# Optimization experiments

Measured on AMD Instinct MI355X. Metric: run time of the kernel, lower is better.

The kernel has to match this reference:

```python
import jax, jax.numpy as jnp
import numpy as np

B, T, C, H, E, K = 4, 2048, 1024, 2048, 8, 2


def setup_inputs() -> dict:
    key = jax.random.key(0)
    ks = jax.random.split(key, 9)
    s = lambda k, shape, fan: jax.random.normal(k, shape, jnp.float32) / np.sqrt(fan)
    return {
        "x": jax.random.normal(ks[0], (B, T, C), jnp.float32),
        "gate_w": s(ks[1], (C, E), C),            # router gate (no bias)
        "sg_w": s(ks[2], (C, H), C),              # shared expert: gate proj
        "su_w": s(ks[3], (C, H), C),              # shared expert: up proj
        "sd_w": s(ks[4], (H, C), H),              # shared expert: down proj
        "eg_w": s(ks[5], (E, C, H), C),           # routed experts: gate proj
        "eu_w": s(ks[6], (E, C, H), C),           # routed experts: up proj
        "ed_w": s(ks[7], (E, H, C), H),           # routed experts: down proj
    }


def _swiglu(x, wg, wu, wd):
    # x: (B,T,C) -> (B,T,C)
    return jnp.einsum("bth,hc->btc", jax.nn.silu(jnp.einsum("btc,ch->bth", x, wg)) * jnp.einsum("btc,ch->bth", x, wu), wd)


def reference(x, gate_w, sg_w, su_w, sd_w, eg_w, eu_w, ed_w):
    # Router: top-k over expert logits, softmax over selected logits
    logits = jnp.einsum("btc,ce->bte", x, gate_w)            # (B,T,E)
    topk_logits, topk_idx = jax.lax.top_k(logits, K)         # (B,T,K)
    weights = jax.nn.softmax(topk_logits, axis=-1)           # (B,T,K)
    # Dense per-expert combine weight: w_e[b,t,e] = sum_k weights*(idx==e)
    onehot = jax.nn.one_hot(topk_idx, E, dtype=x.dtype)      # (B,T,K,E)
    dense_w = jnp.einsum("btk,btke->bte", weights, onehot)   # (B,T,E)

    shared_out = _swiglu(x, sg_w, su_w, sd_w)

    # Scan over experts (small fixed E), accumulating weighted expert outputs.
    dense_w_e = jnp.moveaxis(dense_w, -1, 0)                 # (E,B,T)

    def step(acc, params):
        wg, wu, wd, w = params
        return acc + w[..., None] * _swiglu(x, wg, wu, wd), None

    expert_out, _ = jax.lax.scan(step, jnp.zeros_like(x), (eg_w, eu_w, ed_w, dense_w_e))
    return shared_out + expert_out, logits
```

## Files before the change

kernel.cpp:

```cpp
#include <hip/hip_runtime.h>
#include <cstdint>
#include <cstddef>

#define NTOK 8192
#define CDIM 1024
#define HDIM 2048
#define NEXP 8
#define NSEG 9
#define MAXTILES 104
#define GUTILES (MAXTILES * 2)

typedef __bf16 bf16;
typedef unsigned short u16;
typedef __attribute__((ext_vector_type(8))) __bf16 bf16x8;
typedef __attribute__((ext_vector_type(4))) float f32x4;

__device__ __forceinline__ u16 f2bf(float f) {
  union { u16 u; __bf16 b; } cv;
  cv.b = (__bf16)f;
  return cv.u;
}

__device__ __forceinline__ void gload_lds16(const bf16* g, bf16* l) {
  __builtin_amdgcn_global_load_lds(
      (const __attribute__((address_space(1))) unsigned int*)g,
      (__attribute__((address_space(3))) unsigned int*)l, 16, 0, 0);
}

__global__ __launch_bounds__(64) void init_kernel(int* __restrict__ counts,
                                                  int* __restrict__ fill) {
  if (threadIdx.x < NEXP) {
    counts[threadIdx.x] = 0;
    fill[threadIdx.x] = 0;
  }
}

__global__ __launch_bounds__(256) void zero_out_kernel(float* __restrict__ out) {
  size_t i = ((size_t)blockIdx.x * 256 + threadIdx.x) * 8;
  float4 z = {0.f, 0.f, 0.f, 0.f};
  *(float4*)(out + i) = z;
  *(float4*)(out + i + 4) = z;
}

__global__ __launch_bounds__(256) void cast_x_kernel(
    const float* __restrict__ src, bf16* __restrict__ dst) {
  size_t i = ((size_t)blockIdx.x * 256 + threadIdx.x) * 8;
  float4 a = *(const float4*)(src + i);
  float4 b = *(const float4*)(src + i + 4);
  bf16x8 p;
  p[0] = (bf16)a.x; p[1] = (bf16)a.y; p[2] = (bf16)a.z; p[3] = (bf16)a.w;
  p[4] = (bf16)b.x; p[5] = (bf16)b.y; p[6] = (bf16)b.z; p[7] = (bf16)b.w;
  *(bf16x8*)(dst + i) = p;
}

__global__ __launch_bounds__(256) void router2_kernel(
    const float* __restrict__ x, const float* __restrict__ gw,
    float* __restrict__ logits_out, int* __restrict__ tk_e,
    float* __restrict__ tk_w, int* __restrict__ counts) {
  int wv = threadIdx.x >> 6, l = threadIdx.x & 63;
  int t = blockIdx.x * 4 + wv;
  const float* xr = x + (size_t)t * CDIM;
  float acc[NEXP];
#pragma unroll
  for (int e = 0; e < NEXP; ++e) acc[e] = 0.f;
  for (int c = l; c < CDIM; c += 64) {
    float xv = xr[c];
    const float* g = gw + (size_t)c * NEXP;
    float4 g0 = *(const float4*)(g);
    float4 g1 = *(const float4*)(g + 4);
    acc[0] += xv * g0.x; acc[1] += xv * g0.y; acc[2] += xv * g0.z; acc[3] += xv * g0.w;
    acc[4] += xv * g1.x; acc[5] += xv * g1.y; acc[6] += xv * g1.z; acc[7] += xv * g1.w;
  }
#pragma unroll
  for (int off = 32; off > 0; off >>= 1) {
#pragma unroll
    for (int e = 0; e < NEXP; ++e) acc[e] += __shfl_xor(acc[e], off, 64);
  }
  int e0 = 0; float l0 = acc[0];
#pragma unroll
  for (int e = 1; e < NEXP; ++e) { if (acc[e] > l0) { l0 = acc[e]; e0 = e; } }
  int e1 = -1; float l1 = -3.4e38f;
#pragma unroll
  for (int e = 0; e < NEXP; ++e) { if (e != e0 && acc[e] > l1) { l1 = acc[e]; e1 = e; } }
  float ex = expf(l1 - l0);
  float w0 = 1.f / (1.f + ex), w1 = ex / (1.f + ex);
  if (l < NEXP) logits_out[(size_t)t * NEXP + l] = acc[l];
  if (l == 0) {
    tk_e[2 * t] = e0; tk_e[2 * t + 1] = e1;
    tk_w[2 * t] = w0; tk_w[2 * t + 1] = w1;
    atomicAdd(&counts[e0], 1);
    atomicAdd(&counts[e1], 1);
  }
}

__global__ __launch_bounds__(256) void offsets_kernel(
    const int* __restrict__ counts, int* __restrict__ offs_g,
    int* __restrict__ tile_seg, int* __restrict__ list_tok,
    float* __restrict__ w_row) {
  __shared__ int off[NSEG], pad[NSEG], cnt[NSEG], ntot;
  int tid = threadIdx.x;
  if (tid == 0) {
    int tot = 0;
    for (int e = 0; e < NSEG; ++e) {
      int c = (e < NEXP) ? counts[e] : NTOK;
      cnt[e] = c; off[e] = tot;
      int p = (c + 255) & ~255;
      pad[e] = p; tot += p;
    }
    ntot = tot;
  }
  __syncthreads();
  if (tid < NSEG) offs_g[tid] = off[tid];
  for (int gt = tid; gt < MAXTILES; gt += 256) {
    int row = gt * 256, seg = -1;
    if (row < ntot) {
      for (int e = 0; e < NSEG; ++e)
        if (row >= off[e] && row < off[e] + pad[e]) { seg = e; break; }
    }
    tile_seg[gt] = seg;
  }
  for (int e = 0; e < NSEG; ++e)
    for (int i = off[e] + cnt[e] + tid; i < off[e] + pad[e]; i += 256) {
      list_tok[i] = 0;
      w_row[i] = 0.f;
    }
}

__global__ __launch_bounds__(256) void scatter_kernel(
    const int* __restrict__ tk_e, const float* __restrict__ tk_w,
    const int* __restrict__ offs, int* __restrict__ fill,
    int* __restrict__ list_tok, float* __restrict__ w_row) {
  int t = blockIdx.x * 256 + threadIdx.x;
  int e0 = tk_e[2 * t], e1 = tk_e[2 * t + 1];
  float w0 = tk_w[2 * t], w1 = tk_w[2 * t + 1];
  int p0 = atomicAdd(&fill[e0], 1);
  int i0 = offs[e0] + p0;
  list_tok[i0] = t; w_row[i0] = w0;
  int p1 = atomicAdd(&fill[e1], 1);
  int i1 = offs[e1] + p1;
  list_tok[i1] = t; w_row[i1] = w1;
  int rsh = offs[NEXP] + t;
  list_tok[rsh] = t; w_row[rsh] = 1.f;
}

__device__ __forceinline__ void transpose_body(const float* __restrict__ src,
                                               u16* __restrict__ dst, int R, int C) {
  __shared__ u16 tile[64][65];
  int r0 = blockIdx.y * 64, c0 = blockIdx.x * 64;
  int tr = threadIdx.x >> 2;
  int tc = (threadIdx.x & 3) * 16;
  const float* s = src + (size_t)(r0 + tr) * C + c0 + tc;
  float4 f[4];
#pragma unroll
  for (int q = 0; q < 4; ++q) f[q] = *(const float4*)(s + q * 4);
#pragma unroll
  for (int q = 0; q < 4; ++q) {
    tile[tr][tc + q * 4 + 0] = f2bf(f[q].x);
    tile[tr][tc + q * 4 + 1] = f2bf(f[q].y);
    tile[tr][tc + q * 4 + 2] = f2bf(f[q].z);
    tile[tr][tc + q * 4 + 3] = f2bf(f[q].w);
  }
  __syncthreads();
  union { uint4 v[2]; u16 e[16]; } u;
#pragma unroll
  for (int j = 0; j < 16; ++j) u.e[j] = tile[tc + j][tr];
  u16* d = dst + (size_t)(c0 + tr) * R + r0 + tc;
  *(uint4*)d = u.v[0];
  *(uint4*)(d + 8) = u.v[1];
}

__global__ __launch_bounds__(256) void transpose_cast_kernel(
    const float* __restrict__ src, u16* __restrict__ dst, int R, int C) {
  transpose_body(src, dst, R, C);
}

__global__ __launch_bounds__(256) void transpose_gu_kernel(
    const float* __restrict__ sg, const float* __restrict__ su,
    const float* __restrict__ eg, const float* __restrict__ eu,
    u16* __restrict__ wTg, u16* __restrict__ wTu) {
  const size_t slot = (size_t)HDIM * CDIM;
  int z = blockIdx.z;
  const float* src; u16* dst;
  if (z == 0)       { src = sg;                 dst = wTg + 8 * slot; }
  else if (z == 1)  { src = su;                 dst = wTu + 8 * slot; }
  else if (z < 10)  { src = eg + (z - 2) * slot;  dst = wTg + (z - 2) * slot; }
  else              { src = eu + (z - 10) * slot; dst = wTu + (z - 10) * slot; }
  transpose_body(src, dst, CDIM, HDIM);
}

__global__ __launch_bounds__(256) void transpose_d_kernel(
    const float* __restrict__ sd, const float* __restrict__ ed,
    u16* __restrict__ wTd) {
  const size_t slot = (size_t)HDIM * CDIM;
  int z = blockIdx.z;
  const float* src; u16* dst;
  if (z == 0) { src = sd;                 dst = wTd + 8 * slot; }
  else        { src = ed + (z - 1) * slot; dst = wTd + (z - 1) * slot; }
  transpose_body(src, dst, HDIM, CDIM);
}


__global__ __launch_bounds__(512, 4) void gemm_gu3(
    const bf16* __restrict__ xb, const bf16* __restrict__ wTg,
    const bf16* __restrict__ wTu, const int* __restrict__ tile_seg,
    const int* __restrict__ list_tok, bf16* __restrict__ act) {
  __shared__ __align__(16) bf16 sS[2][12288];
  __shared__ int tokLds[128];

  const int nwg = gridDim.x;
  const int bid = blockIdx.x;
  const int wid = (bid & 7) * (nwg >> 3) + (bid >> 3);
  const int tileIdx = wid % GUTILES;
  const int colIdx = wid / GUTILES;
  const int seg = tile_seg[tileIdx >> 1];
  if (seg < 0) return;

  const int tid = threadIdx.x, l = tid & 63, wv = tid >> 6;
  const int wr = wv >> 2, wn = wv & 3;
  const int n0 = colIdx * 128;
  const size_t rowbase = (size_t)tileIdx * 128;

  if (tid < 128) tokLds[tid] = list_tok[rowbase + tid];
  __syncthreads();

  const int srow = 2 * (tid >> 3) + ((tid >> 2) & 1);
  const int scol = (((tid & 3) ^ ((tid >> 3) & 3)) << 3);
  const bf16* gA = xb + (size_t)tokLds[srow] * CDIM + scol;
  const size_t wslot = (size_t)seg * HDIM * CDIM;
  const bf16* gBg = wTg + wslot + (size_t)(n0 + srow) * CDIM + scol;
  const bf16* gBu = wTu + wslot + (size_t)(n0 + srow) * CDIM + scol;
  const int ldst = tid * 8;

  const int fr = l & 15, u = l >> 4;
  const int laneRd = (fr >> 1) * 128 + (fr & 1) * 64 + ((u ^ ((fr >> 1) & 3)) << 4);
  const int aOff = (wr * 64) * 64 + laneRd;
  const int bOff = (wn * 32) * 64 + laneRd;

  f32x4 accG[4][2], accU[4][2];
#pragma unroll
  for (int i = 0; i < 4; ++i)
#pragma unroll
    for (int j = 0; j < 2; ++j) {
      accG[i][j] = (f32x4){0.f, 0.f, 0.f, 0.f};
      accU[i][j] = (f32x4){0.f, 0.f, 0.f, 0.f};
    }

  auto stage = [&](int b, int k0) {
    bf16* d = &sS[b][0] + ldst;
    gload_lds16(gA + k0, d);
    gload_lds16(gBg + k0, d + 4096);
    gload_lds16(gBu + k0, d + 8192);
  };

  constexpr int NKT = CDIM / 32;
  stage(0, 0);
  stage(1, 32);
  for (int kt = 0; kt < NKT; ++kt) {
    if (kt < NKT - 1) asm volatile("s_waitcnt vmcnt(3)" ::: "memory");
    else              asm volatile("s_waitcnt vmcnt(0)" ::: "memory");
    __builtin_amdgcn_s_barrier();
    const char* pS = (const char*)&sS[kt & 1][0];
    bf16x8 af[4], bg[2], bu[2];
#pragma unroll
    for (int i = 0; i < 4; ++i) af[i] = *(const bf16x8*)(pS + aOff + i * 1024);
#pragma unroll
    for (int j = 0; j < 2; ++j) {
      bg[j] = *(const bf16x8*)(pS + 8192 + bOff + j * 1024);
      bu[j] = *(const bf16x8*)(pS + 16384 + bOff + j * 1024);
    }
    asm volatile("s_waitcnt lgkmcnt(0)" ::: "memory");
    __builtin_amdgcn_s_barrier();
    if (kt + 2 < NKT) stage(kt & 1, (kt + 2) * 32);
    __builtin_amdgcn_s_setprio(1);
#pragma unroll
    for (int i = 0; i < 4; ++i)
#pragma unroll
      for (int j = 0; j < 2; ++j) {
        accG[i][j] = __builtin_amdgcn_mfma_f32_16x16x32_bf16(af[i], bg[j], accG[i][j], 0, 0, 0);
        accU[i][j] = __builtin_amdgcn_mfma_f32_16x16x32_bf16(af[i], bu[j], accU[i][j], 0, 0, 0);
      }
    __builtin_amdgcn_s_setprio(0);
  }

  const int cn = n0 + wn * 32 + fr;
  const int rb = wr * 64 + (l >> 4) * 4;
#pragma unroll
  for (int i = 0; i < 4; ++i)
#pragma unroll
    for (int r = 0; r < 4; ++r) {
      const size_t row = rowbase + rb + i * 16 + r;
#pragma unroll
      for (int j = 0; j < 2; ++j) {
        float g = accG[i][j][r], uu = accU[i][j][r];
        float s = g / (1.f + expf(-g));
        act[row * HDIM + cn + j * 16] = (bf16)(s * uu);
      }
    }
}

__global__ __launch_bounds__(512, 4) void gemm_down3(
    const bf16* __restrict__ act, const bf16* __restrict__ wTd,
    const int* __restrict__ tile_seg, const int* __restrict__ list_tok,
    const float* __restrict__ w_row, float* __restrict__ out) {
  __shared__ __align__(16) bf16 sS[2][12288];
  __shared__ int tokLds[256];
  __shared__ float wLds[256];

  const int nwg = gridDim.x;
  const int bid = blockIdx.x;
  const int wid = (bid & 7) * (nwg >> 3) + (bid >> 3);
  const int tileIdx = wid % MAXTILES;
  const int colIdx = wid / MAXTILES;
  const int seg = tile_seg[tileIdx];
  if (seg < 0) return;

  const int tid = threadIdx.x, l = tid & 63, wv = tid >> 6;
  const int wr = wv >> 1, wc = wv & 1;
  const int n0 = colIdx * 128;
  const size_t rowbase = (size_t)tileIdx * 256;

  if (tid < 256) tokLds[tid] = list_tok[rowbase + tid];
  else           wLds[tid - 256] = w_row[rowbase + tid - 256];
  __syncthreads();

  const int srow = 2 * (tid >> 3) + ((tid >> 2) & 1);
  const int scol = (((tid & 3) ^ ((tid >> 3) & 3)) << 3);
  const bf16* gA0 = act + (rowbase + srow) * HDIM + scol;
  const bf16* gA1 = act + (rowbase + 128 + srow) * HDIM + scol;
  const bf16* gB  = wTd + (size_t)seg * CDIM * HDIM + (size_t)(n0 + srow) * HDIM + scol;
  const int ldst = tid * 8;

  const int fr = l & 15, u = l >> 4;
  const int laneRd = (fr >> 1) * 128 + (fr & 1) * 64 + ((u ^ ((fr >> 1) & 3)) << 4);
  const int aOff = (wr * 64) * 64 + laneRd;
  const int bOff = 16384 + (wc * 64) * 64 + laneRd;

  f32x4 acc[4][4];
#pragma unroll
  for (int i = 0; i < 4; ++i)
#pragma unroll
    for (int j = 0; j < 4; ++j) acc[i][j] = (f32x4){0.f, 0.f, 0.f, 0.f};

  auto stage = [&](int b, int k0) {
    bf16* d = &sS[b][0] + ldst;
    gload_lds16(gA0 + k0, d);
    gload_lds16(gA1 + k0, d + 4096);
    gload_lds16(gB + k0, d + 8192);
  };

  constexpr int NKT = HDIM / 32;
  stage(0, 0);
  stage(1, 32);
  for (int kt = 0; kt < NKT; ++kt) {
    if (kt < NKT - 1) asm volatile("s_waitcnt vmcnt(3)" ::: "memory");
    else              asm volatile("s_waitcnt vmcnt(0)" ::: "memory");
    __builtin_amdgcn_s_barrier();
    const char* pS = (const char*)&sS[kt & 1][0];
    bf16x8 af[4], bf[4];
#pragma unroll
    for (int i = 0; i < 4; ++i) af[i] = *(const bf16x8*)(pS + aOff + i * 1024);
#pragma unroll
    for (int j = 0; j < 4; ++j) bf[j] = *(const bf16x8*)(pS + bOff + j * 1024);
    asm volatile("s_waitcnt lgkmcnt(0)" ::: "memory");
    __builtin_amdgcn_s_barrier();
    if (kt + 2 < NKT) stage(kt & 1, (kt + 2) * 32);
    __builtin_amdgcn_s_setprio(1);
#pragma unroll
    for (int i = 0; i < 4; ++i)
#pragma unroll
      for (int j = 0; j < 4; ++j)
        acc[i][j] = __builtin_amdgcn_mfma_f32_16x16x32_bf16(af[i], bf[j], acc[i][j], 0, 0, 0);
    __builtin_amdgcn_s_setprio(0);
  }

  const int cn = n0 + wc * 64 + fr;
  const int rb = wr * 64 + (l >> 4) * 4;
#pragma unroll
  for (int i = 0; i < 4; ++i)
#pragma unroll
    for (int r = 0; r < 4; ++r) {
      const int lrow = rb + i * 16 + r;
      const float w = wLds[lrow];
      if (w != 0.f) {
        const int tok = tokLds[lrow];
        float* op = out + (size_t)tok * CDIM + cn;
#pragma unroll
        for (int j = 0; j < 4; ++j)
          atomicAdd(op + j * 16, w * acc[i][j][r]);
      }
    }
}

__global__ __launch_bounds__(256) void router_kernel(
    const float* __restrict__ x, const float* __restrict__ gw,
    float* __restrict__ dense_w, float* __restrict__ logits_out) {
  int wv = threadIdx.x >> 6, l = threadIdx.x & 63;
  int t = blockIdx.x * 4 + wv;
  const float* xr = x + (size_t)t * CDIM;
  float acc[NEXP];
#pragma unroll
  for (int e = 0; e < NEXP; ++e) acc[e] = 0.f;
  for (int c = l; c < CDIM; c += 64) {
    float xv = xr[c];
    const float* g = gw + (size_t)c * NEXP;
    float4 g0 = *(const float4*)(g);
    float4 g1 = *(const float4*)(g + 4);
    acc[0] += xv * g0.x; acc[1] += xv * g0.y; acc[2] += xv * g0.z; acc[3] += xv * g0.w;
    acc[4] += xv * g1.x; acc[5] += xv * g1.y; acc[6] += xv * g1.z; acc[7] += xv * g1.w;
  }
#pragma unroll
  for (int off = 32; off > 0; off >>= 1) {
#pragma unroll
    for (int e = 0; e < NEXP; ++e) acc[e] += __shfl_xor(acc[e], off, 64);
  }
  int e0 = 0; float l0 = acc[0];
#pragma unroll
  for (int e = 1; e < NEXP; ++e) { if (acc[e] > l0) { l0 = acc[e]; e0 = e; } }
  int e1 = -1; float l1 = -3.4e38f;
#pragma unroll
  for (int e = 0; e < NEXP; ++e) { if (e != e0 && acc[e] > l1) { l1 = acc[e]; e1 = e; } }
  float ex = expf(l1 - l0);
  float w0 = 1.f / (1.f + ex), w1 = ex / (1.f + ex);
  if (l < NEXP) {
    dense_w[(size_t)t * NEXP + l] = (l == e0) ? w0 : ((l == e1) ? w1 : 0.f);
    logits_out[(size_t)t * NEXP + l] = acc[l];
  }
}

template <int MODE>
__global__ __launch_bounds__(256) void gemm_bt(
    const bf16* __restrict__ A, const bf16* __restrict__ Bt,
    int K, int N,
    bf16* __restrict__ Dbf, const bf16* __restrict__ Gin,
    float* __restrict__ outAcc, const float* __restrict__ denseW, int expertId) {
  __shared__ __align__(16) bf16 sA[128 * 32];
  __shared__ __align__(16) bf16 sB[128 * 32];
  const int tid = threadIdx.x;
  const int l = tid & 63, wv = tid >> 6;
  const int wr = wv >> 1, wc = wv & 1;
  const int m0 = blockIdx.y * 128, n0 = blockIdx.x * 128;
  f32x4 acc[4][4];
#pragma unroll
  for (int i = 0; i < 4; ++i)
#pragma unroll
    for (int j = 0; j < 4; ++j) acc[i][j] = (f32x4){0.f, 0.f, 0.f, 0.f};
  const int srow = wv * 16 + (l >> 2);
  const int scol = (l & 3) * 8;
  const bf16* gA = A + (size_t)(m0 + srow) * K + scol;
  const bf16* gB = Bt + (size_t)(n0 + srow) * K + scol;
  bf16* lA = sA + srow * 32 + scol;
  bf16* lB = sB + srow * 32 + scol;
  const int fr = l & 15, fk = (l >> 4) * 8;
  const bf16* rA = sA + (size_t)(wr * 64 + fr) * 32 + fk;
  const bf16* rB = sB + (size_t)(wc * 64 + fr) * 32 + fk;
  for (int k0 = 0; k0 < K; k0 += 32) {
    __syncthreads();
    gload_lds16(gA, lA);
    gload_lds16(gA + (size_t)64 * K, lA + 64 * 32);
    gload_lds16(gB, lB);
    gload_lds16(gB + (size_t)64 * K, lB + 64 * 32);
    gA += 32; gB += 32;
    __syncthreads();
    bf16x8 af[4], bfr[4];
#pragma unroll
    for (int i = 0; i < 4; ++i) af[i] = *(const bf16x8*)(rA + i * 16 * 32);
#pragma unroll
    for (int j = 0; j < 4; ++j) bfr[j] = *(const bf16x8*)(rB + j * 16 * 32);
#pragma unroll
    for (int i = 0; i < 4; ++i)
#pragma unroll
      for (int j = 0; j < 4; ++j)
        acc[i][j] = __builtin_amdgcn_mfma_f32_16x16x32_bf16(af[i], bfr[j], acc[i][j], 0, 0, 0);
  }
  const int cn = n0 + wc * 64 + (l & 15);
  const int rb = m0 + wr * 64 + (l >> 4) * 4;
#pragma unroll
  for (int i = 0; i < 4; ++i)
#pragma unroll
    for (int r = 0; r < 4; ++r) {
      const int m = rb + i * 16 + r;
#pragma unroll
      for (int j = 0; j < 4; ++j) {
        const int n = cn + j * 16;
        float v = acc[i][j][r];
        if (MODE == 0) {
          Dbf[(size_t)m * N + n] = (bf16)v;
        } else if (MODE == 1) {
          float g = (float)Gin[(size_t)m * N + n];
          float s = g / (1.f + expf(-g));
          Dbf[(size_t)m * N + n] = (bf16)(s * v);
        } else if (MODE == 2) {
          outAcc[(size_t)m * N + n] = v;
        } else {
          float w = denseW[(size_t)m * NEXP + expertId];
          outAcc[(size_t)m * N + n] += w * v;
        }
      }
    }
}

extern "C" void kernel_launch(void* const* d_in, const int* in_sizes, int n_in,
                              void* d_out, int out_size, void* d_ws, size_t ws_size,
                              hipStream_t stream) {
  const float* x    = (const float*)d_in[0];
  const float* gate = (const float*)d_in[1];
  const float* sg   = (const float*)d_in[2];
  const float* su   = (const float*)d_in[3];
  const float* sd   = (const float*)d_in[4];
  const float* eg   = (const float*)d_in[5];
  const float* eu   = (const float*)d_in[6];
  const float* ed   = (const float*)d_in[7];
  float* out    = (float*)d_out;
  float* logits = out + (size_t)NTOK * CDIM;

  const size_t MB = 1u << 20;
  const size_t full_need = 226 * MB;

  if (ws_size >= full_need) {
    char* ws = (char*)d_ws;
    bf16*  xb   = (bf16*)(ws);
    bf16*  wTg  = (bf16*)(ws + 16 * MB);
    bf16*  wTu  = (bf16*)(ws + 52 * MB);
    bf16*  act  = (bf16*)(ws + 88 * MB);
    bf16*  wTd  = (bf16*)(ws + 16 * MB);
    char*  sm   = ws + 224 * MB;
    int*   list_tok = (int*)(sm);
    int*   tk_e     = (int*)(sm + 256 * 1024);
    float* tk_w     = (float*)(sm + 320 * 1024);
    int*   tile_seg = (int*)(sm + 384 * 1024);
    int*   counts   = (int*)(sm + 388 * 1024);
    int*   fill     = (int*)(sm + 389 * 1024);
    int*   offs     = (int*)(sm + 390 * 1024);
    float* w_row    = (float*)(sm + 400 * 1024);

    init_kernel<<<1, 64, 0, stream>>>(counts, fill);
    zero_out_kernel<<<NTOK * CDIM / (256 * 8), 256, 0, stream>>>(out);
    cast_x_kernel<<<NTOK * CDIM / (256 * 8), 256, 0, stream>>>(x, xb);
    router2_kernel<<<NTOK / 4, 256, 0, stream>>>(x, gate, logits, tk_e, tk_w, counts);
    offsets_kernel<<<1, 256, 0, stream>>>(counts, offs, tile_seg, list_tok, w_row);
    scatter_kernel<<<NTOK / 256, 256, 0, stream>>>(tk_e, tk_w, offs, fill, list_tok, w_row);

    dim3 tgu(HDIM / 64, CDIM / 64, 18);
    transpose_gu_kernel<<<tgu, 256, 0, stream>>>(sg, su, eg, eu, (u16*)wTg, (u16*)wTu);

    gemm_gu3<<<(HDIM / 128) * GUTILES, 512, 0, stream>>>(xb, wTg, wTu, tile_seg, list_tok, act);

    dim3 tdd(CDIM / 64, HDIM / 64, 9);
    transpose_d_kernel<<<tdd, 256, 0, stream>>>(sd, ed, (u16*)wTd);

    gemm_down3<<<(CDIM / 128) * MAXTILES, 512, 0, stream>>>(act, wTd, tile_seg, list_tok, w_row, out);
    return;
  }

  char* ws = (char*)d_ws;
  bf16*  xb   = (bf16*)(ws);
  bf16*  wTgf = (bf16*)(ws + 16 * MB);
  bf16*  wTuf = (bf16*)(ws + 20 * MB);
  bf16*  wTdf = (bf16*)(ws + 24 * MB);
  bf16*  gbuf = (bf16*)(ws + 28 * MB);
  float* dw   = (float*)(ws + 60 * MB);
  if (ws_size < 60 * MB + (size_t)NTOK * NEXP * sizeof(float)) return;

  cast_x_kernel<<<NTOK * CDIM / (256 * 8), 256, 0, stream>>>(x, xb);
  router_kernel<<<NTOK / 4, 256, 0, stream>>>(x, gate, dw, logits);

  dim3 tg1(HDIM / 64, CDIM / 64);
  dim3 tg2(CDIM / 64, HDIM / 64);
  dim3 g1(HDIM / 128, NTOK / 128);
  dim3 g2(CDIM / 128, NTOK / 128);

  transpose_cast_kernel<<<tg1, 256, 0, stream>>>(sg, (u16*)wTgf, CDIM, HDIM);
  transpose_cast_kernel<<<tg1, 256, 0, stream>>>(su, (u16*)wTuf, CDIM, HDIM);
  transpose_cast_kernel<<<tg2, 256, 0, stream>>>(sd, (u16*)wTdf, HDIM, CDIM);
  gemm_bt<0><<<g1, 256, 0, stream>>>(xb, wTgf, CDIM, HDIM, gbuf, nullptr, nullptr, nullptr, 0);
  gemm_bt<1><<<g1, 256, 0, stream>>>(xb, wTuf, CDIM, HDIM, gbuf, gbuf, nullptr, nullptr, 0);
  gemm_bt<2><<<g2, 256, 0, stream>>>(gbuf, wTdf, HDIM, CDIM, nullptr, nullptr, out, nullptr, 0);

  for (int e = 0; e < NEXP; ++e) {
    const float* egp = eg + (size_t)e * CDIM * HDIM;
    const float* eup = eu + (size_t)e * CDIM * HDIM;
    const float* edp = ed + (size_t)e * HDIM * CDIM;
    transpose_cast_kernel<<<tg1, 256, 0, stream>>>(egp, (u16*)wTgf, CDIM, HDIM);
    transpose_cast_kernel<<<tg1, 256, 0, stream>>>(eup, (u16*)wTuf, CDIM, HDIM);
    transpose_cast_kernel<<<tg2, 256, 0, stream>>>(edp, (u16*)wTdf, HDIM, CDIM);
    gemm_bt<0><<<g1, 256, 0, stream>>>(xb, wTgf, CDIM, HDIM, gbuf, nullptr, nullptr, nullptr, 0);
    gemm_bt<1><<<g1, 256, 0, stream>>>(xb, wTuf, CDIM, HDIM, gbuf, gbuf, nullptr, nullptr, 0);
    gemm_bt<3><<<g2, 256, 0, stream>>>(gbuf, wTdf, HDIM, CDIM, nullptr, nullptr, out, dw, e);
  }
}
```

Measured before the change: 970.6 us.

## Enlarge GEMM tiles to 256 rows with BK=64 and phased MFMA/load interleave

```diff
diff --git a/kernel.cpp b/kernel.cpp
--- a/kernel.cpp
+++ b/kernel.cpp
@@ -8,7 +8,6 @@
 #define NEXP 8
 #define NSEG 9
 #define MAXTILES 104
-#define GUTILES (MAXTILES * 2)
 
 typedef __bf16 bf16;
 typedef unsigned short u16;
@@ -200,111 +199,12 @@
 }
 
 
-__global__ __launch_bounds__(512, 4) void gemm_gu3(
+__global__ __launch_bounds__(512, 2) void gemm_gu4(
     const bf16* __restrict__ xb, const bf16* __restrict__ wTg,
     const bf16* __restrict__ wTu, const int* __restrict__ tile_seg,
     const int* __restrict__ list_tok, bf16* __restrict__ act) {
-  __shared__ __align__(16) bf16 sS[2][12288];
-  __shared__ int tokLds[128];
-
-  const int nwg = gridDim.x;
-  const int bid = blockIdx.x;
-  const int wid = (bid & 7) * (nwg >> 3) + (bid >> 3);
-  const int tileIdx = wid % GUTILES;
-  const int colIdx = wid / GUTILES;
-  const int seg = tile_seg[tileIdx >> 1];
-  if (seg < 0) return;
-
-  const int tid = threadIdx.x, l = tid & 63, wv = tid >> 6;
-  const int wr = wv >> 2, wn = wv & 3;
-  const int n0 = colIdx * 128;
-  const size_t rowbase = (size_t)tileIdx * 128;
-
-  if (tid < 128) tokLds[tid] = list_tok[rowbase + tid];
-  __syncthreads();
-
-  const int srow = 2 * (tid >> 3) + ((tid >> 2) & 1);
-  const int scol = (((tid & 3) ^ ((tid >> 3) & 3)) << 3);
-  const bf16* gA = xb + (size_t)tokLds[srow] * CDIM + scol;
-  const size_t wslot = (size_t)seg * HDIM * CDIM;
-  const bf16* gBg = wTg + wslot + (size_t)(n0 + srow) * CDIM + scol;
-  const bf16* gBu = wTu + wslot + (size_t)(n0 + srow) * CDIM + scol;
-  const int ldst = tid * 8;
-
-  const int fr = l & 15, u = l >> 4;
-  const int laneRd = (fr >> 1) * 128 + (fr & 1) * 64 + ((u ^ ((fr >> 1) & 3)) << 4);
-  const int aOff = (wr * 64) * 64 + laneRd;
-  const int bOff = (wn * 32) * 64 + laneRd;
-
-  f32x4 accG[4][2], accU[4][2];
-#pragma unroll
-  for (int i = 0; i < 4; ++i)
-#pragma unroll
-    for (int j = 0; j < 2; ++j) {
-      accG[i][j] = (f32x4){0.f, 0.f, 0.f, 0.f};
-      accU[i][j] = (f32x4){0.f, 0.f, 0.f, 0.f};
-    }
-
-  auto stage = [&](int b, int k0) {
-    bf16* d = &sS[b][0] + ldst;
-    gload_lds16(gA + k0, d);
-    gload_lds16(gBg + k0, d + 4096);
-    gload_lds16(gBu + k0, d + 8192);
-  };
-
-  constexpr int NKT = CDIM / 32;
-  stage(0, 0);
-  stage(1, 32);
-  for (int kt = 0; kt < NKT; ++kt) {
-    if (kt < NKT - 1) asm volatile("s_waitcnt vmcnt(3)" ::: "memory");
-    else              asm volatile("s_waitcnt vmcnt(0)" ::: "memory");
-    __builtin_amdgcn_s_barrier();
-    const char* pS = (const char*)&sS[kt & 1][0];
-    bf16x8 af[4], bg[2], bu[2];
-#pragma unroll
-    for (int i = 0; i < 4; ++i) af[i] = *(const bf16x8*)(pS + aOff + i * 1024);
-#pragma unroll
-    for (int j = 0; j < 2; ++j) {
-      bg[j] = *(const bf16x8*)(pS + 8192 + bOff + j * 1024);
-      bu[j] = *(const bf16x8*)(pS + 16384 + bOff + j * 1024);
-    }
-    asm volatile("s_waitcnt lgkmcnt(0)" ::: "memory");
-    __builtin_amdgcn_s_barrier();
-    if (kt + 2 < NKT) stage(kt & 1, (kt + 2) * 32);
-    __builtin_amdgcn_s_setprio(1);
-#pragma unroll
-    for (int i = 0; i < 4; ++i)
-#pragma unroll
-      for (int j = 0; j < 2; ++j) {
-        accG[i][j] = __builtin_amdgcn_mfma_f32_16x16x32_bf16(af[i], bg[j], accG[i][j], 0, 0, 0);
-        accU[i][j] = __builtin_amdgcn_mfma_f32_16x16x32_bf16(af[i], bu[j], accU[i][j], 0, 0, 0);
-      }
-    __builtin_amdgcn_s_setprio(0);
-  }
-
-  const int cn = n0 + wn * 32 + fr;
-  const int rb = wr * 64 + (l >> 4) * 4;
-#pragma unroll
-  for (int i = 0; i < 4; ++i)
-#pragma unroll
-    for (int r = 0; r < 4; ++r) {
-      const size_t row = rowbase + rb + i * 16 + r;
-#pragma unroll
-      for (int j = 0; j < 2; ++j) {
-        float g = accG[i][j][r], uu = accU[i][j][r];
-        float s = g / (1.f + expf(-g));
-        act[row * HDIM + cn + j * 16] = (bf16)(s * uu);
-      }
-    }
-}
-
-__global__ __launch_bounds__(512, 4) void gemm_down3(
-    const bf16* __restrict__ act, const bf16* __restrict__ wTd,
-    const int* __restrict__ tile_seg, const int* __restrict__ list_tok,
-    const float* __restrict__ w_row, float* __restrict__ out) {
-  __shared__ __align__(16) bf16 sS[2][12288];
+  __shared__ __align__(16) bf16 sS[2][32768];
   __shared__ int tokLds[256];
-  __shared__ float wLds[256];
 
   const int nwg = gridDim.x;
   const int bid = blockIdx.x;
@@ -315,7 +215,181 @@
   if (seg < 0) return;
 
   const int tid = threadIdx.x, l = tid & 63, wv = tid >> 6;
-  const int wr = wv >> 1, wc = wv & 1;
+  const int wr = wv >> 2, wn = wv & 3;
+  const int n0 = colIdx * 128;
+  const size_t rowbase = (size_t)tileIdx * 256;
+
+  if (tid < 256) tokLds[tid] = list_tok[rowbase + tid];
+  __syncthreads();
+
+  const int row8 = tid >> 3;
+  const int scol = (((tid & 7) ^ (row8 & 7)) << 3);
+  const bf16* gA0 = xb + (size_t)tokLds[row8] * CDIM + scol;
+  const bf16* gA1 = xb + (size_t)tokLds[128 + row8] * CDIM + scol;
+  const bf16* gA2 = xb + (size_t)tokLds[64 + row8] * CDIM + scol;
+  const bf16* gA3 = xb + (size_t)tokLds[192 + row8] * CDIM + scol;
+  const size_t wslot = (size_t)seg * HDIM * CDIM;
+  const bf16* gBg = wTg + wslot + (size_t)(n0 + row8) * CDIM + scol;
+  const bf16* gBu = wTu + wslot + (size_t)(n0 + row8) * CDIM + scol;
+  const int t8 = tid * 8;
+
+  const int fr = l & 15, kq = l >> 4;
+  const int cS0 = ((kq ^ (l & 7)) << 4);
+  const int cS1 = (((4 | kq) ^ (l & 7)) << 4);
+  const int aBase = (wr * 128 + fr) * 128;
+  const int gBase = 32768 + (wn * 32 + fr) * 128;
+  const int uBase = 49152 + (wn * 32 + fr) * 128;
+
+  f32x4 accG[2][4][2], accU[2][4][2];
+#pragma unroll
+  for (int h = 0; h < 2; ++h)
+#pragma unroll
+    for (int i = 0; i < 4; ++i)
+#pragma unroll
+      for (int j = 0; j < 2; ++j) {
+        accG[h][i][j] = (f32x4){0.f, 0.f, 0.f, 0.f};
+        accU[h][i][j] = (f32x4){0.f, 0.f, 0.f, 0.f};
+      }
+
+  auto stC0 = [&](int b, int k0) { bf16* d = &sS[b][0];
+    gload_lds16(gBg + k0, d + 16384 + t8);
+    gload_lds16(gBg + 64 * CDIM + k0, d + 20480 + t8); };
+  auto stC1 = [&](int b, int k0) { bf16* d = &sS[b][0];
+    gload_lds16(gA0 + k0, d + t8);
+    gload_lds16(gA1 + k0, d + 8192 + t8); };
+  auto stC2 = [&](int b, int k0) { bf16* d = &sS[b][0];
+    gload_lds16(gBu + k0, d + 24576 + t8);
+    gload_lds16(gBu + 64 * CDIM + k0, d + 28672 + t8); };
+  auto stC3 = [&](int b, int k0) { bf16* d = &sS[b][0];
+    gload_lds16(gA2 + k0, d + 4096 + t8);
+    gload_lds16(gA3 + k0, d + 12288 + t8); };
+
+  constexpr int NKT = CDIM / 64;
+  stC0(0, 0); stC1(0, 0); stC2(0, 0); stC3(0, 0);
+
+  for (int kt = 0; kt < NKT; ++kt) {
+    const int b = kt & 1, bn = b ^ 1;
+    const int kn = (kt + 1) * 64;
+    const bool more = (kt + 1 < NKT);
+    const char* pS = (const char*)&sS[b][0];
+    bf16x8 af[4][2], bg[2][2], bu[2][2];
+
+    asm volatile("s_waitcnt vmcnt(4)" ::: "memory");
+    __builtin_amdgcn_s_barrier();
+#pragma unroll
+    for (int i = 0; i < 4; ++i) {
+      af[i][0] = *(const bf16x8*)(pS + aBase + i * 2048 + cS0);
+      af[i][1] = *(const bf16x8*)(pS + aBase + i * 2048 + cS1);
+    }
+#pragma unroll
+    for (int j = 0; j < 2; ++j) {
+      bg[j][0] = *(const bf16x8*)(pS + gBase + j * 2048 + cS0);
+      bg[j][1] = *(const bf16x8*)(pS + gBase + j * 2048 + cS1);
+    }
+    if (more) stC0(bn, kn);
+    asm volatile("s_waitcnt lgkmcnt(0)" ::: "memory");
+    __builtin_amdgcn_sched_barrier(0);
+    __builtin_amdgcn_s_setprio(1);
+#pragma unroll
+    for (int i = 0; i < 4; ++i)
+#pragma unroll
+      for (int j = 0; j < 2; ++j) {
+        accG[0][i][j] = __builtin_amdgcn_mfma_f32_16x16x32_bf16(af[i][0], bg[j][0], accG[0][i][j], 0, 0, 0);
+        accG[0][i][j] = __builtin_amdgcn_mfma_f32_16x16x32_bf16(af[i][1], bg[j][1], accG[0][i][j], 0, 0, 0);
+      }
+    __builtin_amdgcn_s_setprio(0);
+
+    if (more) asm volatile("s_waitcnt vmcnt(4)" ::: "memory");
+    else      asm volatile("s_waitcnt vmcnt(2)" ::: "memory");
+    __builtin_amdgcn_s_barrier();
+#pragma unroll
+    for (int j = 0; j < 2; ++j) {
+      bu[j][0] = *(const bf16x8*)(pS + uBase + j * 2048 + cS0);
+      bu[j][1] = *(const bf16x8*)(pS + uBase + j * 2048 + cS1);
+    }
+    if (more) stC1(bn, kn);
+    asm volatile("s_waitcnt lgkmcnt(0)" ::: "memory");
+    __builtin_amdgcn_sched_barrier(0);
+    __builtin_amdgcn_s_setprio(1);
+#pragma unroll
+    for (int i = 0; i < 4; ++i)
+#pragma unroll
+      for (int j = 0; j < 2; ++j) {
+        accU[0][i][j] = __builtin_amdgcn_mfma_f32_16x16x32_bf16(af[i][0], bu[j][0], accU[0][i][j], 0, 0, 0);
+        accU[0][i][j] = __builtin_amdgcn_mfma_f32_16x16x32_bf16(af[i][1], bu[j][1], accU[0][i][j], 0, 0, 0);
+      }
+    __builtin_amdgcn_s_setprio(0);
+
+    if (more) asm volatile("s_waitcnt vmcnt(4)" ::: "memory");
+    else      asm volatile("s_waitcnt vmcnt(0)" ::: "memory");
+    __builtin_amdgcn_s_barrier();
+#pragma unroll
+    for (int i = 0; i < 4; ++i) {
+      af[i][0] = *(const bf16x8*)(pS + aBase + 8192 + i * 2048 + cS0);
+      af[i][1] = *(const bf16x8*)(pS + aBase + 8192 + i * 2048 + cS1);
+    }
+    if (more) stC2(bn, kn);
+    asm volatile("s_waitcnt lgkmcnt(0)" ::: "memory");
+    __builtin_amdgcn_sched_barrier(0);
+    __builtin_amdgcn_s_setprio(1);
+#pragma unroll
+    for (int i = 0; i < 4; ++i)
+#pragma unroll
+      for (int j = 0; j < 2; ++j) {
+        accG[1][i][j] = __builtin_amdgcn_mfma_f32_16x16x32_bf16(af[i][0], bg[j][0], accG[1][i][j], 0, 0, 0);
+        accG[1][i][j] = __builtin_amdgcn_mfma_f32_16x16x32_bf16(af[i][1], bg[j][1], accG[1][i][j], 0, 0, 0);
+      }
+    __builtin_amdgcn_s_setprio(0);
+
+    __builtin_amdgcn_s_barrier();
+    if (more) stC3(bn, kn);
+    __builtin_amdgcn_s_setprio(1);
+#pragma unroll
+    for (int i = 0; i < 4; ++i)
+#pragma unroll
+      for (int j = 0; j < 2; ++j) {
+        accU[1][i][j] = __builtin_amdgcn_mfma_f32_16x16x32_bf16(af[i][0], bu[j][0], accU[1][i][j], 0, 0, 0);
+        accU[1][i][j] = __builtin_amdgcn_mfma_f32_16x16x32_bf16(af[i][1], bu[j][1], accU[1][i][j], 0, 0, 0);
+      }
+    __builtin_amdgcn_s_setprio(0);
+  }
+
+  const int cn = n0 + wn * 32 + fr;
+  const int rb = wr * 128 + kq * 4;
+#pragma unroll
+  for (int h = 0; h < 2; ++h)
+#pragma unroll
+    for (int i = 0; i < 4; ++i)
+#pragma unroll
+      for (int r = 0; r < 4; ++r) {
+        const size_t row = rowbase + rb + h * 64 + i * 16 + r;
+#pragma unroll
+        for (int j = 0; j < 2; ++j) {
+          float g = accG[h][i][j][r], uu = accU[h][i][j][r];
+          float s = g / (1.f + expf(-g));
+          act[row * HDIM + cn + j * 16] = (bf16)(s * uu);
+        }
+      }
+}
+
+__global__ __launch_bounds__(512, 2) void gemm_down4(
+    const bf16* __restrict__ act, const bf16* __restrict__ wTd,
+    const int* __restrict__ tile_seg, const int* __restrict__ list_tok,
+    const float* __restrict__ w_row, float* __restrict__ out) {
+  __shared__ __align__(16) bf16 sS[2][24576];
+  __shared__ int tokLds[256];
+  __shared__ float wLds[256];
+
+  const int nwg = gridDim.x;
+  const int bid = blockIdx.x;
+  const int wid = (bid & 7) * (nwg >> 3) + (bid >> 3);
+  const int tileIdx = wid % MAXTILES;
+  const int colIdx = wid / MAXTILES;
+  const int seg = tile_seg[tileIdx];
+  if (seg < 0) return;
+
+  const int tid = threadIdx.x, l = tid & 63, wv = tid >> 6;
+  const int wr = wv >> 2, wn = wv & 3;
   const int n0 = colIdx * 128;
   const size_t rowbase = (size_t)tileIdx * 256;
 
@@ -323,72 +397,114 @@
   else           wLds[tid - 256] = w_row[rowbase + tid - 256];
   __syncthreads();
 
-  const int srow = 2 * (tid >> 3) + ((tid >> 2) & 1);
-  const int scol = (((tid & 3) ^ ((tid >> 3) & 3)) << 3);
-  const bf16* gA0 = act + (rowbase + srow) * HDIM + scol;
-  const bf16* gA1 = act + (rowbase + 128 + srow) * HDIM + scol;
-  const bf16* gB  = wTd + (size_t)seg * CDIM * HDIM + (size_t)(n0 + srow) * HDIM + scol;
-  const int ldst = tid * 8;
-
-  const int fr = l & 15, u = l >> 4;
-  const int laneRd = (fr >> 1) * 128 + (fr & 1) * 64 + ((u ^ ((fr >> 1) & 3)) << 4);
-  const int aOff = (wr * 64) * 64 + laneRd;
-  const int bOff = 16384 + (wc * 64) * 64 + laneRd;
-
-  f32x4 acc[4][4];
-#pragma unroll
-  for (int i = 0; i < 4; ++i)
-#pragma unroll
-    for (int j = 0; j < 4; ++j) acc[i][j] = (f32x4){0.f, 0.f, 0.f, 0.f};
-
-  auto stage = [&](int b, int k0) {
-    bf16* d = &sS[b][0] + ldst;
-    gload_lds16(gA0 + k0, d);
-    gload_lds16(gA1 + k0, d + 4096);
-    gload_lds16(gB + k0, d + 8192);
-  };
-
-  constexpr int NKT = HDIM / 32;
-  stage(0, 0);
-  stage(1, 32);
+  const int row8 = tid >> 3;
+  const int scol = (((tid & 7) ^ (row8 & 7)) << 3);
+  const bf16* gA0 = act + (rowbase + row8) * HDIM + scol;
+  const bf16* gA1 = act + (rowbase + 128 + row8) * HDIM + scol;
+  const bf16* gA2 = act + (rowbase + 64 + row8) * HDIM + scol;
+  const bf16* gA3 = act + (rowbase + 192 + row8) * HDIM + scol;
+  const bf16* gB  = wTd + (size_t)seg * CDIM * HDIM + (size_t)(n0 + row8) * HDIM + scol;
+  const int t8 = tid * 8;
+
+  const int fr = l & 15, kq = l >> 4;
+  const int cS0 = ((kq ^ (l & 7)) << 4);
+  const int cS1 = (((4 | kq) ^ (l & 7)) << 4);
+  const int aBase = (wr * 128 + fr) * 128;
+  const int bBase = 32768 + (wn * 32 + fr) * 128;
+
+  f32x4 acc[2][4][2];
+#pragma unroll
+  for (int h = 0; h < 2; ++h)
+#pragma unroll
+    for (int i = 0; i < 4; ++i)
+#pragma unroll
+      for (int j = 0; j < 2; ++j) acc[h][i][j] = (f32x4){0.f, 0.f, 0.f, 0.f};
+
+  auto stC0 = [&](int b, int k0) { bf16* d = &sS[b][0];
+    gload_lds16(gB + k0, d + 16384 + t8);
+    gload_lds16(gB + 64 * HDIM + k0, d + 20480 + t8); };
+  auto stC1 = [&](int b, int k0) { bf16* d = &sS[b][0];
+    gload_lds16(gA0 + k0, d + t8);
+    gload_lds16(gA1 + k0, d + 8192 + t8); };
+  auto stC2 = [&](int b, int k0) { bf16* d = &sS[b][0];
+    gload_lds16(gA2 + k0, d + 4096 + t8);
+    gload_lds16(gA3 + k0, d + 12288 + t8); };
+
+  constexpr int NKT = HDIM / 64;
+  stC0(0, 0); stC1(0, 0); stC2(0, 0);
+
   for (int kt = 0; kt < NKT; ++kt) {
-    if (kt < NKT - 1) asm volatile("s_waitcnt vmcnt(3)" ::: "memory");
-    else              asm volatile("s_waitcnt vmcnt(0)" ::: "memory");
+    const int b = kt & 1, bn = b ^ 1;
+    const int kn = (kt + 1) * 64;
+    const bool more = (kt + 1 < NKT);
+    const char* pS = (const char*)&sS[b][0];
+    bf16x8 af[4][2], bf[2][2];
+
+    asm volatile("s_waitcnt vmcnt(2)" ::: "memory");
     __builtin_amdgcn_s_barrier();
-    const char* pS = (const char*)&sS[kt & 1][0];
-    bf16x8 af[4], bf[4];
-#pragma unroll
-    for (int i = 0; i < 4; ++i) af[i] = *(const bf16x8*)(pS + aOff + i * 1024);
-#pragma unroll
-    for (int j = 0; j < 4; ++j) bf[j] = *(const bf16x8*)(pS + bOff + j * 1024);
+#pragma unroll
+    for (int i = 0; i < 4; ++i) {
+      af[i][0] = *(const bf16x8*)(pS + aBase + i * 2048 + cS0);
+      af[i][1] = *(const bf16x8*)(pS + aBase + i * 2048 + cS1);
+    }
+#pragma unroll
+    for (int j = 0; j < 2; ++j) {
+      bf[j][0] = *(const bf16x8*)(pS + bBase + j * 2048 + cS0);
+      bf[j][1] = *(const bf16x8*)(pS + bBase + j * 2048 + cS1);
+    }
+    if (more) { stC0(bn, kn); stC1(bn, kn); }
     asm volatile("s_waitcnt lgkmcnt(0)" ::: "memory");
+    __builtin_amdgcn_sched_barrier(0);
+    __builtin_amdgcn_s_setprio(1);
+#pragma unroll
+    for (int i = 0; i < 4; ++i)
+#pragma unroll
+      for (int j = 0; j < 2; ++j) {
+        acc[0][i][j] = __builtin_amdgcn_mfma_f32_16x16x32_bf16(af[i][0], bf[j][0], acc[0][i][j], 0, 0, 0);
+        acc[0][i][j] = __builtin_amdgcn_mfma_f32_16x16x32_bf16(af[i][1], bf[j][1], acc[0][i][j], 0, 0, 0);
+      }
+    __builtin_amdgcn_s_setprio(0);
+
+    if (more) asm volatile("s_waitcnt vmcnt(4)" ::: "memory");
+    else      asm volatile("s_waitcnt vmcnt(0)" ::: "memory");
     __builtin_amdgcn_s_barrier();
-    if (kt + 2 < NKT) stage(kt & 1, (kt + 2) * 32);
+#pragma unroll
+    for (int i = 0; i < 4; ++i) {
+      af[i][0] = *(const bf16x8*)(pS + aBase + 8192 + i * 2048 + cS0);
+      af[i][1] = *(const bf16x8*)(pS + aBase + 8192 + i * 2048 + cS1);
+    }
+    if (more) stC2(bn, kn);
+    asm volatile("s_waitcnt lgkmcnt(0)" ::: "memory");
+    __builtin_amdgcn_sched_barrier(0);
     __builtin_amdgcn_s_setprio(1);
 #pragma unroll
     for (int i = 0; i < 4; ++i)
 #pragma unroll
-      for (int j = 0; j < 4; ++j)
-        acc[i][j] = __builtin_amdgcn_mfma_f32_16x16x32_bf16(af[i], bf[j], acc[i][j], 0, 0, 0);
+      for (int j = 0; j < 2; ++j) {
+        acc[1][i][j] = __builtin_amdgcn_mfma_f32_16x16x32_bf16(af[i][0], bf[j][0], acc[1][i][j], 0, 0, 0);
+        acc[1][i][j] = __builtin_amdgcn_mfma_f32_16x16x32_bf16(af[i][1], bf[j][1], acc[1][i][j], 0, 0, 0);
+      }
     __builtin_amdgcn_s_setprio(0);
   }
 
-  const int cn = n0 + wc * 64 + fr;
-  const int rb = wr * 64 + (l >> 4) * 4;
-#pragma unroll
-  for (int i = 0; i < 4; ++i)
-#pragma unroll
-    for (int r = 0; r < 4; ++r) {
-      const int lrow = rb + i * 16 + r;
-      const float w = wLds[lrow];
-      if (w != 0.f) {
-        const int tok = tokLds[lrow];
-        float* op = out + (size_t)tok * CDIM + cn;
-#pragma unroll
-        for (int j = 0; j < 4; ++j)
-          atomicAdd(op + j * 16, w * acc[i][j][r]);
-      }
-    }
+  const int cn = n0 + wn * 32 + fr;
+  const int rb = wr * 128 + kq * 4;
+#pragma unroll
+  for (int h = 0; h < 2; ++h)
+#pragma unroll
+    for (int i = 0; i < 4; ++i)
+#pragma unroll
+      for (int r = 0; r < 4; ++r) {
+        const int lrow = rb + h * 64 + i * 16 + r;
+        const float w = wLds[lrow];
+        if (w != 0.f) {
+          const int tok = tokLds[lrow];
+          float* op = out + (size_t)tok * CDIM + cn;
+#pragma unroll
+          for (int j = 0; j < 2; ++j)
+            atomicAdd(op + j * 16, w * acc[h][i][j][r]);
+        }
+      }
 }
 
 __global__ __launch_bounds__(256) void router_kernel(
@@ -543,12 +659,12 @@
     dim3 tgu(HDIM / 64, CDIM / 64, 18);
     transpose_gu_kernel<<<tgu, 256, 0, stream>>>(sg, su, eg, eu, (u16*)wTg, (u16*)wTu);
 
-    gemm_gu3<<<(HDIM / 128) * GUTILES, 512, 0, stream>>>(xb, wTg, wTu, tile_seg, list_tok, act);
+    gemm_gu4<<<(HDIM / 128) * MAXTILES, 512, 0, stream>>>(xb, wTg, wTu, tile_seg, list_tok, act);
 
     dim3 tdd(CDIM / 64, HDIM / 64, 9);
     transpose_d_kernel<<<tdd, 256, 0, stream>>>(sd, ed, (u16*)wTd);
 
-    gemm_down3<<<(CDIM / 128) * MAXTILES, 512, 0, stream>>>(act, wTd, tile_seg, list_tok, w_row, out);
+    gemm_down4<<<(CDIM / 128) * MAXTILES, 512, 0, stream>>>(act, wTd, tile_seg, list_tok, w_row, out);
     return;
   }
 
```

After: 969.1 us. About the same (-0.2%).
